# Kernel optimization log

Measured on AMD Instinct MI355X. Metric: run time of the kernel, lower is better.

The kernel has to match this reference:

```python
import jax, jax.numpy as jnp
import numpy as np

N_NODES = 100000
N_EDGES = 1600000
N_QUERY = 200000
IN_CH = 128
HID = 64


def setup_inputs() -> dict:
    key = jax.random.key(0)
    ks = jax.random.split(key, 8)
    x = jax.random.normal(ks[0], (N_NODES, IN_CH), dtype=jnp.float32)
    edge_index = jax.random.randint(ks[1], (2, N_EDGES), 0, N_NODES, dtype=jnp.int64)
    src = jax.random.randint(ks[2], (N_QUERY,), 0, N_NODES, dtype=jnp.int64)
    dst = jax.random.randint(ks[3], (N_QUERY,), 0, N_NODES, dtype=jnp.int64)
    # SAGEConv params: lin_l (neighbor path, with bias), lin_r (root path, no bias)
    s1 = 1.0 / np.sqrt(IN_CH)
    s2 = 1.0 / np.sqrt(HID)
    Wl1 = jax.random.normal(ks[4], (HID, IN_CH), dtype=jnp.float32) * s1
    bl1 = jnp.zeros((HID,), dtype=jnp.float32)
    Wr1 = jax.random.normal(ks[5], (HID, IN_CH), dtype=jnp.float32) * s1
    Wl2 = jax.random.normal(ks[6], (HID, HID), dtype=jnp.float32) * s2
    bl2 = jnp.zeros((HID,), dtype=jnp.float32)
    Wr2 = jax.random.normal(ks[7], (HID, HID), dtype=jnp.float32) * s2
    return {"x": x, "edge_index": edge_index, "src": src, "dst": dst,
            "Wl1": Wl1, "bl1": bl1, "Wr1": Wr1,
            "Wl2": Wl2, "bl2": bl2, "Wr2": Wr2}


def _sage_conv(h, edge_src, edge_dst, Wl, bl, Wr, num_nodes):
    # mean aggregation of source-node features onto destination nodes
    msg_sum = jax.ops.segment_sum(h[edge_src], edge_dst, num_segments=num_nodes)  # [N, F]
    cnt = jax.ops.segment_sum(jnp.ones((edge_src.shape[0], 1), h.dtype), edge_dst,
                              num_segments=num_nodes)  # [N, 1]
    agg = msg_sum / jnp.maximum(cnt, 1.0)
    return agg @ Wl.T + bl + h @ Wr.T


def reference(x, edge_index, src, dst, Wl1, bl1, Wr1, Wl2, bl2, Wr2):
    n = x.shape[0]
    e_src, e_dst = edge_index[0], edge_index[1]
    h = jax.nn.relu(_sage_conv(x, e_src, e_dst, Wl1, bl1, Wr1, n))
    z = jax.nn.relu(_sage_conv(h, e_src, e_dst, Wl2, bl2, Wr2, n))
    return jax.nn.sigmoid(jnp.sum(z[src] * z[dst], axis=-1))
```

## Files before the change

### kernel.cpp

```cpp
#include <hip/hip_runtime.h>
#include <hip/hip_bf16.h>
#include <math.h>


#define HID 64
#define G_BLK 512
#define NB_MAX 512

typedef __attribute__((ext_vector_type(8))) short short8;
typedef __attribute__((ext_vector_type(4))) float floatx4;

__device__ __forceinline__ unsigned short f2bf(float f) {
    union { float f; unsigned u; } v; v.f = f;
    unsigned r = v.u + 0x7FFF + ((v.u >> 16) & 1);
    return (unsigned short)(r >> 16);
}
__device__ __forceinline__ float bf2f(unsigned short u) {
    union { unsigned u; float f; } v; v.u = ((unsigned)u) << 16;
    return v.f;
}
__device__ __forceinline__ unsigned pack_bf2(float a, float b) {
    union { __hip_bfloat162 h; unsigned u; } cv;
    cv.h = __float22bfloat162_rn(make_float2(a, b));
    return cv.u;
}
__device__ __forceinline__ void acc8(float* a, uint4 u) {
    a[0] += bf2f((unsigned short)u.x); a[1] += bf2f((unsigned short)(u.x >> 16));
    a[2] += bf2f((unsigned short)u.y); a[3] += bf2f((unsigned short)(u.y >> 16));
    a[4] += bf2f((unsigned short)u.z); a[5] += bf2f((unsigned short)(u.z >> 16));
    a[6] += bf2f((unsigned short)u.w); a[7] += bf2f((unsigned short)(u.w >> 16));
}


__global__ __launch_bounds__(256)
void k_bhist(const int* __restrict__ edst, int* __restrict__ cnt,
             int E, int NB, int CH) {
    __shared__ int lh[NB_MAX];
    const int b = blockIdx.x;
    for (int i = threadIdx.x; i < NB; i += 256) lh[i] = 0;
    __syncthreads();
    const int e0 = b * CH;
    const int e1 = min(E, e0 + CH);
    for (int e = e0 + threadIdx.x; e < e1; e += 256)
        atomicAdd(&lh[edst[e] >> 8], 1);
    __syncthreads();
    for (int k = threadIdx.x; k < NB; k += 256)
        cnt[(size_t)k * G_BLK + b] = lh[k];
}

__global__ __launch_bounds__(256)
void k_bscan1(int* __restrict__ cnt, int* __restrict__ total, int NB) {
    int k = blockIdx.x * 4 + (threadIdx.x >> 6);
    int lane = threadIdx.x & 63;
    if (k >= NB) return;
    int* row = cnt + (size_t)k * G_BLK;
    const int base = lane * 8;
    int v[8];
#pragma unroll
    for (int j = 0; j < 8; ++j) v[j] = row[base + j];
    int s = 0;
#pragma unroll
    for (int j = 0; j < 8; ++j) s += v[j];
    int inc = s;
#pragma unroll
    for (int off = 1; off < 64; off <<= 1) {
        int o = __shfl_up(inc, off, 64);
        if (lane >= off) inc += o;
    }
    int run = inc - s;
#pragma unroll
    for (int j = 0; j < 8; ++j) { int t = v[j]; row[base + j] = run; run += t; }
    if (lane == 63) total[k] = run;
}

__global__ __launch_bounds__(512)
void k_bscan2(const int* __restrict__ total, int* __restrict__ base, int NB) {
    __shared__ int lds[512];
    int t = threadIdx.x;
    int v = (t < NB) ? total[t] : 0;
    lds[t] = v;
    __syncthreads();
    for (int off = 1; off < 512; off <<= 1) {
        int x = (t >= off) ? lds[t - off] : 0;
        __syncthreads();
        lds[t] += x;
        __syncthreads();
    }
    if (t < NB) base[t] = lds[t] - v;
}

__global__ __launch_bounds__(256)
void k_bscatter(const int* __restrict__ esrc, const int* __restrict__ edst,
                const int* __restrict__ cnt, const int* __restrict__ base,
                int* __restrict__ ebuf, int E, int NB, int CH) {
    __shared__ int cur[NB_MAX];
    const int b = blockIdx.x;
    for (int k = threadIdx.x; k < NB; k += 256)
        cur[k] = base[k] + cnt[(size_t)k * G_BLK + b];
    __syncthreads();
    const int e0 = b * CH;
    const int e1 = min(E, e0 + CH);
    for (int e = e0 + threadIdx.x; e < e1; e += 256) {
        int d = edst[e];
        int slot = atomicAdd(&cur[d >> 8], 1);
        ebuf[slot] = ((d & 255) << 24) | esrc[e];
    }
}

__global__ __launch_bounds__(256)
void k_bfinal(const int* __restrict__ ebuf, const int* __restrict__ total,
              const int* __restrict__ base, int* __restrict__ sorted,
              int* __restrict__ deg, int* __restrict__ offs, int N) {
    __shared__ int h[256], loc[256], cur[256], sc[256];
    const int k = blockIdx.x;
    const int t = threadIdx.x;
    const int nk = total[k];
    const int bs = base[k];
    h[t] = 0;
    __syncthreads();
    for (int i = bs + t; i < bs + nk; i += 256)
        atomicAdd(&h[(ebuf[i] >> 24) & 255], 1);
    __syncthreads();
    int v = h[t];
    sc[t] = v;
    __syncthreads();
    for (int off = 1; off < 256; off <<= 1) {
        int x = (t >= off) ? sc[t - off] : 0;
        __syncthreads();
        sc[t] += x;
        __syncthreads();
    }
    loc[t] = sc[t] - v;
    cur[t] = sc[t] - v;
    __syncthreads();
    for (int i = bs + t; i < bs + nk; i += 256) {
        int pk = ebuf[i];
        int j = (pk >> 24) & 255;
        int r = atomicAdd(&cur[j], 1);
        sorted[bs + r] = pk & 0xFFFFFF;
    }
    int node = (k << 8) + t;
    if (node < N) {
        deg[node] = v;
        offs[node] = bs + loc[t];
    }
}


__global__ __launch_bounds__(256)
void k_castw(const float* __restrict__ Wl1, const float* __restrict__ Wr1,
             const float* __restrict__ Wl2, const float* __restrict__ Wr2,
             unsigned short* __restrict__ Wcb1, unsigned short* __restrict__ Wcb2) {
    int i = blockIdx.x * 256 + threadIdx.x;
    if (i < 16384) {
        Wcb1[i] = f2bf(i < 8192 ? Wl1[i] : Wr1[i - 8192]);
    } else if (i < 24576) {
        int j = i - 16384;
        Wcb2[j] = f2bf(j < 4096 ? Wl2[j] : Wr2[j - 4096]);
    }
}


template <int K, bool AF32>
__global__ __launch_bounds__(256, 2)
void gemm_mfma(const void* __restrict__ Xv, const unsigned short* __restrict__ Wcb,
               unsigned short* __restrict__ Pb, float* __restrict__ Qc, int N) {
    const int lane = threadIdx.x & 63;
    const int m = lane & 15;
    const int q = lane >> 4;
    const int gw = blockIdx.x * 4 + (threadIdx.x >> 6);
    const int half = gw & 1;
    constexpr int KB = K / 32;

    short8 bf[KB][4];
#pragma unroll
    for (int kb = 0; kb < KB; ++kb)
#pragma unroll
        for (int ct = 0; ct < 4; ++ct) {
            int c = half * 64 + ct * 16 + m;
            bf[kb][ct] = *(const short8*)(Wcb + (size_t)c * K + kb * 32 + q * 8);
        }

    const int ntiles = (N + 15) >> 4;
    const int stride = gridDim.x * 2;
    for (int t = gw >> 1; t < ntiles; t += stride) {
        const int r0 = t << 4;
        int rr = r0 + m;
        if (rr >= N) rr = N - 1;
        floatx4 acc[4];
#pragma unroll
        for (int ct = 0; ct < 4; ++ct) acc[ct] = (floatx4){0.f, 0.f, 0.f, 0.f};

#pragma unroll
        for (int kb = 0; kb < KB; ++kb) {
            short8 a;
            if (AF32) {
                const float* xp = (const float*)Xv + (size_t)rr * K + kb * 32 + q * 8;
                float4 x0 = *(const float4*)xp;
                float4 x1 = *(const float4*)(xp + 4);
                union { unsigned u[4]; short8 s; } cv;
                cv.u[0] = pack_bf2(x0.x, x0.y);
                cv.u[1] = pack_bf2(x0.z, x0.w);
                cv.u[2] = pack_bf2(x1.x, x1.y);
                cv.u[3] = pack_bf2(x1.z, x1.w);
                a = cv.s;
            } else {
                a = *(const short8*)((const unsigned short*)Xv + (size_t)rr * K + kb * 32 + q * 8);
            }
#pragma unroll
            for (int ct = 0; ct < 4; ++ct)
                acc[ct] = __builtin_amdgcn_mfma_f32_16x16x32_bf16(a, bf[kb][ct], acc[ct], 0, 0, 0);
        }

#pragma unroll
        for (int i = 0; i < 4; ++i) {
            int row = r0 + q * 4 + i;
            if (row < N) {
                if (half == 0) {
#pragma unroll
                    for (int ct = 0; ct < 4; ++ct)
                        Pb[(size_t)row * HID + ct * 16 + m] = f2bf(acc[ct][i]);
                } else {
#pragma unroll
                    for (int ct = 0; ct < 4; ++ct)
                        Qc[(size_t)row * HID + ct * 16 + m] = acc[ct][i];
                }
            }
        }
    }
}


__global__ __launch_bounds__(256)
void k_agg(const uint4* __restrict__ P8, const float4* __restrict__ Qin4,
           const float4* __restrict__ bias4, const int* __restrict__ offs,
           const int* __restrict__ deg, const int* __restrict__ sorted,
           uint4* __restrict__ H8, int N) {
    int node = blockIdx.x * 32 + (threadIdx.x >> 3);
    int c8 = threadIdx.x & 7;
    if (node >= N) return;
    int off = offs[node];
    int c = deg[node];
    float a[8];
#pragma unroll
    for (int j = 0; j < 8; ++j) a[j] = 0.f;
    int i = 0;
    for (; i + 1 < c; i += 2) {
        int s0 = sorted[off + i];
        int s1 = sorted[off + i + 1];
        uint4 u0 = P8[(size_t)s0 * 8 + c8];
        uint4 u1 = P8[(size_t)s1 * 8 + c8];
        acc8(a, u0);
        acc8(a, u1);
    }
    if (i < c) acc8(a, P8[(size_t)sorted[off + i] * 8 + c8]);

    float inv = 1.0f / (float)(c > 0 ? c : 1);
    float4 b0 = bias4[c8 * 2], b1 = bias4[c8 * 2 + 1];
    float4 q0 = Qin4[(size_t)node * 16 + c8 * 2];
    float4 q1 = Qin4[(size_t)node * 16 + c8 * 2 + 1];
    float v0 = a[0] * inv + b0.x + q0.x;
    float v1 = a[1] * inv + b0.y + q0.y;
    float v2 = a[2] * inv + b0.z + q0.z;
    float v3 = a[3] * inv + b0.w + q0.w;
    float v4 = a[4] * inv + b1.x + q1.x;
    float v5 = a[5] * inv + b1.y + q1.y;
    float v6 = a[6] * inv + b1.z + q1.z;
    float v7 = a[7] * inv + b1.w + q1.w;
    v0 = fmaxf(v0, 0.f); v1 = fmaxf(v1, 0.f); v2 = fmaxf(v2, 0.f); v3 = fmaxf(v3, 0.f);
    v4 = fmaxf(v4, 0.f); v5 = fmaxf(v5, 0.f); v6 = fmaxf(v6, 0.f); v7 = fmaxf(v7, 0.f);
    uint4 hp;
    hp.x = (unsigned)f2bf(v0) | ((unsigned)f2bf(v1) << 16);
    hp.y = (unsigned)f2bf(v2) | ((unsigned)f2bf(v3) << 16);
    hp.z = (unsigned)f2bf(v4) | ((unsigned)f2bf(v5) << 16);
    hp.w = (unsigned)f2bf(v6) | ((unsigned)f2bf(v7) << 16);
    H8[(size_t)node * 8 + c8] = hp;
}


__global__ __launch_bounds__(256)
void k_query(const uint4* __restrict__ Z8, const int* __restrict__ src,
             const int* __restrict__ dst, float* __restrict__ out, int Q) {
    int qi = blockIdx.x * 32 + (threadIdx.x >> 3);
    int c8 = threadIdx.x & 7;
    if (qi >= Q) return;
    int s = src[qi];
    int d = dst[qi];
    uint4 us = Z8[(size_t)s * 8 + c8];
    uint4 ud = Z8[(size_t)d * 8 + c8];
    float v =
        bf2f((unsigned short)us.x) * bf2f((unsigned short)ud.x) +
        bf2f((unsigned short)(us.x >> 16)) * bf2f((unsigned short)(ud.x >> 16)) +
        bf2f((unsigned short)us.y) * bf2f((unsigned short)ud.y) +
        bf2f((unsigned short)(us.y >> 16)) * bf2f((unsigned short)(ud.y >> 16)) +
        bf2f((unsigned short)us.z) * bf2f((unsigned short)ud.z) +
        bf2f((unsigned short)(us.z >> 16)) * bf2f((unsigned short)(ud.z >> 16)) +
        bf2f((unsigned short)us.w) * bf2f((unsigned short)ud.w) +
        bf2f((unsigned short)(us.w >> 16)) * bf2f((unsigned short)(ud.w >> 16));
#pragma unroll
    for (int mres = 4; mres > 0; mres >>= 1) v += __shfl_xor(v, mres, 64);
    if (c8 == 0) out[qi] = 1.0f / (1.0f + __expf(-v));
}


extern "C" void kernel_launch(void* const* d_in, const int* in_sizes, int n_in,
                              void* d_out, int out_size, void* d_ws, size_t ws_size,
                              hipStream_t stream) {
    const float* x    = (const float*)d_in[0];
    const int*   ei   = (const int*)d_in[1];
    const int*   qsrc = (const int*)d_in[2];
    const int*   qdst = (const int*)d_in[3];
    const float* Wl1  = (const float*)d_in[4];
    const float* bl1  = (const float*)d_in[5];
    const float* Wr1  = (const float*)d_in[6];
    const float* Wl2  = (const float*)d_in[7];
    const float* bl2  = (const float*)d_in[8];
    const float* Wr2  = (const float*)d_in[9];
    float* out = (float*)d_out;

    const int N = in_sizes[0] / 128;
    const int E = in_sizes[1] / 2;
    const int Q = in_sizes[2];

    const int* esrc = ei;
    const int* edst = ei + E;

    float*          Qc  = (float*)d_ws;
    unsigned short* Pb  = (unsigned short*)(Qc + (size_t)N * HID);
    unsigned short* Hb  = Pb + (size_t)N * HID;
    unsigned short* Zb  = Hb + (size_t)N * HID;
    int* deg_c  = (int*)(Zb + (size_t)N * HID);
    int* offs   = deg_c + N;
    int* total  = offs + N;
    int* base   = total + NB_MAX;
    int* sorted = base + NB_MAX;
    unsigned short* Wcb1 = (unsigned short*)(sorted + E);
    unsigned short* Wcb2 = Wcb1 + 16384;
    int* cnt  = (int*)Qc;
    int* ebuf = (int*)Pb;

    const int NB = (N + 255) >> 8;
    const int CH = (E + G_BLK - 1) / G_BLK;
    const int gG = 640;
    const int gA = (N + 31) / 32;
    const int gQ = (Q + 31) / 32;

    k_castw<<<96, 256, 0, stream>>>(Wl1, Wr1, Wl2, Wr2, Wcb1, Wcb2);
    k_bhist<<<G_BLK, 256, 0, stream>>>(edst, cnt, E, NB, CH);
    k_bscan1<<<(NB + 3) / 4, 256, 0, stream>>>(cnt, total, NB);
    k_bscan2<<<1, 512, 0, stream>>>(total, base, NB);
    k_bscatter<<<G_BLK, 256, 0, stream>>>(esrc, edst, cnt, base, ebuf, E, NB, CH);
    k_bfinal<<<NB, 256, 0, stream>>>(ebuf, total, base, sorted, deg_c, offs, N);

    gemm_mfma<128, true><<<gG, 256, 0, stream>>>(x, Wcb1, Pb, Qc, N);
    k_agg<<<gA, 256, 0, stream>>>((const uint4*)Pb, (const float4*)Qc,
                                  (const float4*)bl1, offs, deg_c, sorted,
                                  (uint4*)Hb, N);

    gemm_mfma<64, false><<<gG, 256, 0, stream>>>(Hb, Wcb2, Pb, Qc, N);
    k_agg<<<gA, 256, 0, stream>>>((const uint4*)Pb, (const float4*)Qc,
                                  (const float4*)bl2, offs, deg_c, sorted,
                                  (uint4*)Zb, N);

    k_query<<<gQ, 256, 0, stream>>>((const uint4*)Zb, qsrc, qdst, out, Q);
}
```

Baseline: 260.2 us.

## Store root-path projection as bf16, fuse weight cast into GEMM, widen histogram grid

The root-path GEMM output Q is now written as bf16 instead of fp32, which halves its write traffic and its read traffic in the aggregation kernel. The separate weight-cast kernel is removed: each GEMM wave converts its fp32 weight slice to bf16 in registers. The edge histogram and scatter grid doubles to 1024 blocks, and the scan kernel now handles 16 entries per lane. The workspace layout changes so cnt and ebuf get their own regions instead of aliasing the Q and P buffers. The cost is extra rounding error on Q.

Result: no change. 264.1 us (+1.5%).

```diff
diff --git a/kernel.cpp b/kernel.cpp
--- a/kernel.cpp
+++ b/kernel.cpp
@@ -4,7 +4,7 @@
 
 
 #define HID 64
-#define G_BLK 512
+#define G_BLK 1024
 #define NB_MAX 512
 
 typedef __attribute__((ext_vector_type(8))) short short8;
@@ -54,13 +54,13 @@
     int lane = threadIdx.x & 63;
     if (k >= NB) return;
     int* row = cnt + (size_t)k * G_BLK;
-    const int base = lane * 8;
-    int v[8];
-#pragma unroll
-    for (int j = 0; j < 8; ++j) v[j] = row[base + j];
+    const int base = lane * 16;
+    int v[16];
+#pragma unroll
+    for (int j = 0; j < 16; ++j) v[j] = row[base + j];
     int s = 0;
 #pragma unroll
-    for (int j = 0; j < 8; ++j) s += v[j];
+    for (int j = 0; j < 16; ++j) s += v[j];
     int inc = s;
 #pragma unroll
     for (int off = 1; off < 64; off <<= 1) {
@@ -69,7 +69,7 @@
     }
     int run = inc - s;
 #pragma unroll
-    for (int j = 0; j < 8; ++j) { int t = v[j]; row[base + j] = run; run += t; }
+    for (int j = 0; j < 16; ++j) { int t = v[j]; row[base + j] = run; run += t; }
     if (lane == 63) total[k] = run;
 }
 
@@ -147,24 +147,11 @@
 }
 
 
-__global__ __launch_bounds__(256)
-void k_castw(const float* __restrict__ Wl1, const float* __restrict__ Wr1,
-             const float* __restrict__ Wl2, const float* __restrict__ Wr2,
-             unsigned short* __restrict__ Wcb1, unsigned short* __restrict__ Wcb2) {
-    int i = blockIdx.x * 256 + threadIdx.x;
-    if (i < 16384) {
-        Wcb1[i] = f2bf(i < 8192 ? Wl1[i] : Wr1[i - 8192]);
-    } else if (i < 24576) {
-        int j = i - 16384;
-        Wcb2[j] = f2bf(j < 4096 ? Wl2[j] : Wr2[j - 4096]);
-    }
-}
-
-
 template <int K, bool AF32>
 __global__ __launch_bounds__(256, 2)
-void gemm_mfma(const void* __restrict__ Xv, const unsigned short* __restrict__ Wcb,
-               unsigned short* __restrict__ Pb, float* __restrict__ Qc, int N) {
+void gemm_mfma(const void* __restrict__ Xv, const float* __restrict__ Wl,
+               const float* __restrict__ Wr, unsigned short* __restrict__ Pb,
+               unsigned short* __restrict__ Qb, int N) {
     const int lane = threadIdx.x & 63;
     const int m = lane & 15;
     const int q = lane >> 4;
@@ -172,15 +159,25 @@
     const int half = gw & 1;
     constexpr int KB = K / 32;
 
+    const float* Wh = half ? Wr : Wl;
     short8 bf[KB][4];
 #pragma unroll
     for (int kb = 0; kb < KB; ++kb)
 #pragma unroll
         for (int ct = 0; ct < 4; ++ct) {
-            int c = half * 64 + ct * 16 + m;
-            bf[kb][ct] = *(const short8*)(Wcb + (size_t)c * K + kb * 32 + q * 8);
+            int c = ct * 16 + m;
+            const float* wp = Wh + (size_t)c * K + kb * 32 + q * 8;
+            float4 w0 = *(const float4*)wp;
+            float4 w1 = *(const float4*)(wp + 4);
+            union { unsigned u[4]; short8 s; } cv;
+            cv.u[0] = pack_bf2(w0.x, w0.y);
+            cv.u[1] = pack_bf2(w0.z, w0.w);
+            cv.u[2] = pack_bf2(w1.x, w1.y);
+            cv.u[3] = pack_bf2(w1.z, w1.w);
+            bf[kb][ct] = cv.s;
         }
 
+    unsigned short* dstp = half ? Qb : Pb;
     const int ntiles = (N + 15) >> 4;
     const int stride = gridDim.x * 2;
     for (int t = gw >> 1; t < ntiles; t += stride) {
@@ -216,15 +213,9 @@
         for (int i = 0; i < 4; ++i) {
             int row = r0 + q * 4 + i;
             if (row < N) {
-                if (half == 0) {
-#pragma unroll
-                    for (int ct = 0; ct < 4; ++ct)
-                        Pb[(size_t)row * HID + ct * 16 + m] = f2bf(acc[ct][i]);
-                } else {
-#pragma unroll
-                    for (int ct = 0; ct < 4; ++ct)
-                        Qc[(size_t)row * HID + ct * 16 + m] = acc[ct][i];
-                }
+#pragma unroll
+                for (int ct = 0; ct < 4; ++ct)
+                    dstp[(size_t)row * HID + ct * 16 + m] = f2bf(acc[ct][i]);
             }
         }
     }
@@ -232,7 +223,7 @@
 
 
 __global__ __launch_bounds__(256)
-void k_agg(const uint4* __restrict__ P8, const float4* __restrict__ Qin4,
+void k_agg(const uint4* __restrict__ P8, const uint2* __restrict__ Qb4,
            const float4* __restrict__ bias4, const int* __restrict__ offs,
            const int* __restrict__ deg, const int* __restrict__ sorted,
            uint4* __restrict__ H8, int N) {
@@ -257,16 +248,16 @@
 
     float inv = 1.0f / (float)(c > 0 ? c : 1);
     float4 b0 = bias4[c8 * 2], b1 = bias4[c8 * 2 + 1];
-    float4 q0 = Qin4[(size_t)node * 16 + c8 * 2];
-    float4 q1 = Qin4[(size_t)node * 16 + c8 * 2 + 1];
-    float v0 = a[0] * inv + b0.x + q0.x;
-    float v1 = a[1] * inv + b0.y + q0.y;
-    float v2 = a[2] * inv + b0.z + q0.z;
-    float v3 = a[3] * inv + b0.w + q0.w;
-    float v4 = a[4] * inv + b1.x + q1.x;
-    float v5 = a[5] * inv + b1.y + q1.y;
-    float v6 = a[6] * inv + b1.z + q1.z;
-    float v7 = a[7] * inv + b1.w + q1.w;
+    uint2 q0 = Qb4[(size_t)node * 16 + c8 * 2];
+    uint2 q1 = Qb4[(size_t)node * 16 + c8 * 2 + 1];
+    float v0 = a[0] * inv + b0.x + bf2f((unsigned short)q0.x);
+    float v1 = a[1] * inv + b0.y + bf2f((unsigned short)(q0.x >> 16));
+    float v2 = a[2] * inv + b0.z + bf2f((unsigned short)q0.y);
+    float v3 = a[3] * inv + b0.w + bf2f((unsigned short)(q0.y >> 16));
+    float v4 = a[4] * inv + b1.x + bf2f((unsigned short)q1.x);
+    float v5 = a[5] * inv + b1.y + bf2f((unsigned short)(q1.x >> 16));
+    float v6 = a[6] * inv + b1.z + bf2f((unsigned short)q1.y);
+    float v7 = a[7] * inv + b1.w + bf2f((unsigned short)(q1.y >> 16));
     v0 = fmaxf(v0, 0.f); v1 = fmaxf(v1, 0.f); v2 = fmaxf(v2, 0.f); v3 = fmaxf(v3, 0.f);
     v4 = fmaxf(v4, 0.f); v5 = fmaxf(v5, 0.f); v6 = fmaxf(v6, 0.f); v7 = fmaxf(v7, 0.f);
     uint4 hp;
@@ -325,19 +316,17 @@
     const int* esrc = ei;
     const int* edst = ei + E;
 
-    float*          Qc  = (float*)d_ws;
-    unsigned short* Pb  = (unsigned short*)(Qc + (size_t)N * HID);
-    unsigned short* Hb  = Pb + (size_t)N * HID;
-    unsigned short* Zb  = Hb + (size_t)N * HID;
+    unsigned short* Pb = (unsigned short*)d_ws;
+    unsigned short* Qb = Pb + (size_t)N * HID;
+    unsigned short* Hb = Qb + (size_t)N * HID;
+    unsigned short* Zb = Hb + (size_t)N * HID;
     int* deg_c  = (int*)(Zb + (size_t)N * HID);
     int* offs   = deg_c + N;
     int* total  = offs + N;
     int* base   = total + NB_MAX;
     int* sorted = base + NB_MAX;
-    unsigned short* Wcb1 = (unsigned short*)(sorted + E);
-    unsigned short* Wcb2 = Wcb1 + 16384;
-    int* cnt  = (int*)Qc;
-    int* ebuf = (int*)Pb;
+    int* cnt    = sorted + E;
+    int* ebuf   = cnt + (size_t)NB_MAX * G_BLK;
 
     const int NB = (N + 255) >> 8;
     const int CH = (E + G_BLK - 1) / G_BLK;
@@ -345,20 +334,19 @@
     const int gA = (N + 31) / 32;
     const int gQ = (Q + 31) / 32;
 
-    k_castw<<<96, 256, 0, stream>>>(Wl1, Wr1, Wl2, Wr2, Wcb1, Wcb2);
     k_bhist<<<G_BLK, 256, 0, stream>>>(edst, cnt, E, NB, CH);
     k_bscan1<<<(NB + 3) / 4, 256, 0, stream>>>(cnt, total, NB);
     k_bscan2<<<1, 512, 0, stream>>>(total, base, NB);
     k_bscatter<<<G_BLK, 256, 0, stream>>>(esrc, edst, cnt, base, ebuf, E, NB, CH);
     k_bfinal<<<NB, 256, 0, stream>>>(ebuf, total, base, sorted, deg_c, offs, N);
 
-    gemm_mfma<128, true><<<gG, 256, 0, stream>>>(x, Wcb1, Pb, Qc, N);
-    k_agg<<<gA, 256, 0, stream>>>((const uint4*)Pb, (const float4*)Qc,
+    gemm_mfma<128, true><<<gG, 256, 0, stream>>>(x, Wl1, Wr1, Pb, Qb, N);
+    k_agg<<<gA, 256, 0, stream>>>((const uint4*)Pb, (const uint2*)Qb,
                                   (const float4*)bl1, offs, deg_c, sorted,
                                   (uint4*)Hb, N);
 
-    gemm_mfma<64, false><<<gG, 256, 0, stream>>>(Hb, Wcb2, Pb, Qc, N);
-    k_agg<<<gA, 256, 0, stream>>>((const uint4*)Pb, (const float4*)Qc,
+    gemm_mfma<64, false><<<gG, 256, 0, stream>>>(Hb, Wl2, Wr2, Pb, Qb, N);
+    k_agg<<<gA, 256, 0, stream>>>((const uint4*)Pb, (const uint2*)Qb,
                                   (const float4*)bl2, offs, deg_c, sorted,
                                   (uint4*)Zb, N);
 
```
